# Kernel tuning notes

Measured on AMD Instinct MI355X. Metric: run time of the kernel, lower is better.

The kernel has to match this reference:

```python
import jax, jax.numpy as jnp
import numpy as np

H_HEADS = 4

def setup_inputs() -> dict:
    key = jax.random.key(0)
    ks = jax.random.split(key, 14)
    B, C, H, W = 8, 512, 32, 32
    r = C // H_HEADS  # SE reduction = h per SelfModule(channel, h)
    s_in = 0.02
    inp = {
        'x': jax.random.normal(ks[0], (B, C, H, W), jnp.float32),
        'wq': jax.random.normal(ks[1], (C, C), jnp.float32) * s_in,
        'bq': jnp.zeros((C,), jnp.float32),
        'wk': jax.random.normal(ks[2], (C, C), jnp.float32) * s_in,
        'bk': jnp.zeros((C,), jnp.float32),
        'wv': jax.random.normal(ks[3], (C, C), jnp.float32) * s_in,
        'bv': jnp.zeros((C,), jnp.float32),
        'fc1_w': jax.random.normal(ks[4], (r, C), jnp.float32) * s_in,
        'fc1_b': jnp.zeros((r,), jnp.float32),
        'fc2_w': jax.random.normal(ks[5], (C, r), jnp.float32) * s_in,
        'fc2_b': jnp.zeros((C,), jnp.float32),
        'gate_w': jax.random.normal(ks[6], (1, C), jnp.float32) * s_in,
        'gate_b': jnp.zeros((1,), jnp.float32),
    }
    return inp

def _conv1x1(y, w, b):
    # y: [B,C,H,W], w: [O,C] (1x1 conv kernel squeezed), b: [O]
    return jnp.einsum('bchw,oc->bohw', y, w) + b[None, :, None, None]

def reference(x, wq, bq, wk, bk, wv, bv, fc1_w, fc1_b, fc2_w, fc2_b, gate_w, gate_b):
    B, C, H, W = x.shape
    h = H_HEADS
    dk = C // h
    N = H * W

    # --- SelfScaling (SE without final sigmoid-in-block; sigmoid applied at mul) ---
    p = x.mean(axis=(2, 3))                                   # [B,C] global avg pool
    f = jax.nn.relu(p @ fc1_w.T + fc1_b) @ fc2_w.T + fc2_b    # [B,C]
    x = x * jax.nn.sigmoid(f)[:, :, None, None] + x

    # --- RTrans: conv1x1 QKV, attention over flattened H*W ---
    q = _conv1x1(x, wq, bq).reshape(B, h, dk, N).transpose(0, 1, 3, 2)  # [B,h,N,dk]
    k = _conv1x1(x, wk, bk).reshape(B, h, dk, N)                        # [B,h,dk,N]
    v = _conv1x1(x, wv, bv).reshape(B, h, dk, N)                        # [B,h,dk,N]
    scale = 1.0 / float(np.sqrt(dk))
    att = jax.nn.softmax(jnp.einsum('bhnd,bhdm->bhnm', q, k) * scale, axis=-1)  # [B,h,N,N]
    o = jnp.einsum('bhdn,bhnm->bhdm', v, att).reshape(B, C, H, W)  # v @ att as in torch

    # --- SelfGating ---
    gate = jax.nn.sigmoid(_conv1x1(o, gate_w, gate_b))  # [B,1,H,W]
    return o * gate + o
```

## Files before the change

### kernel.cpp

```cpp
#include <hip/hip_runtime.h>
#include <hip/hip_bf16.h>

#define B_ 8
#define C_ 512
#define N_ 1024
#define HEADS_ 4
#define DK_ 128
#define R_ 128

typedef float f32x4 __attribute__((ext_vector_type(4)));
typedef __bf16 bf16x8 __attribute__((ext_vector_type(8)));
typedef short short4v __attribute__((ext_vector_type(4)));
typedef unsigned short u16;

constexpr float kScale = 0.08838834764831845f;

#define OFF_P   0u
#define OFF_SS  16384u
#define OFF_WB  32768u
#define OFF_XT  1605632u
#define OFF_QT  9994240u
#define OFF_KT  18382848u
#define OFF_V   26771456u
#define OFF_DEN 35160064u
#define OFF_G   35291136u
#define OFF_O1  35323904u
#define OFF_E   52101120u

__device__ __forceinline__ u16 f2b(float f) {
  __hip_bfloat16 h = __float2bfloat16(f);
  return __builtin_bit_cast(u16, h);
}
__device__ __forceinline__ float b2f(u16 u) {
  return __builtin_bit_cast(float, (unsigned)u << 16);
}

typedef const __attribute__((address_space(1))) unsigned int* gptr_t;
typedef __attribute__((address_space(3))) unsigned int* lptr_t;
__device__ __forceinline__ void gload16(const void* g, void* l) {
  __builtin_amdgcn_global_load_lds((gptr_t)g, (lptr_t)l, 16, 0, 0);
}

__device__ __forceinline__ f32x4 mfma16(bf16x8 a, bf16x8 b, f32x4 c) {
  return __builtin_amdgcn_mfma_f32_16x16x32_bf16(a, b, c, 0, 0, 0);
}

__global__ __launch_bounds__(64) void k_pool(const float* __restrict__ x,
                                             float* __restrict__ p) {
  int bc = blockIdx.x, lane = threadIdx.x;
  const float4* row = (const float4*)(x + (size_t)bc * N_);
  float s = 0.f;
  for (int i = lane; i < N_ / 4; i += 64) {
    float4 t = row[i];
    s += t.x + t.y + t.z + t.w;
  }
  for (int o = 32; o > 0; o >>= 1) s += __shfl_down(s, o, 64);
  if (lane == 0) p[bc] = s * (1.0f / N_);
}

__global__ __launch_bounds__(256) void k_se(const float* __restrict__ p,
                                            const float* __restrict__ fc1w,
                                            const float* __restrict__ fc1b,
                                            const float* __restrict__ fc2w,
                                            const float* __restrict__ fc2b,
                                            float* __restrict__ ss) {
  __shared__ float pl[C_];
  __shared__ float f1[R_];
  int b = blockIdx.x, t = threadIdx.x;
  for (int c = t; c < C_; c += 256) pl[c] = p[b * C_ + c];
  __syncthreads();
  if (t < R_) {
    float a = fc1b[t];
    for (int c = 0; c < C_; c++) a += pl[c] * fc1w[t * C_ + c];
    f1[t] = fmaxf(a, 0.f);
  }
  __syncthreads();
  for (int c = t; c < C_; c += 256) {
    float a = fc2b[c];
    for (int j = 0; j < R_; j++) a += f1[j] * fc2w[c * R_ + j];
    ss[b * C_ + c] = 1.f + 1.f / (1.f + __expf(-a));
  }
}

__global__ __launch_bounds__(256) void k_castw_zero(const float* __restrict__ wq,
                                                    const float* __restrict__ wk,
                                                    const float* __restrict__ wv,
                                                    u16* __restrict__ wb,
                                                    float* __restrict__ g) {
  int bid = blockIdx.x;
  if (bid >= 768) {
    g[(bid - 768) * 256 + threadIdx.x] = 0.f;
    return;
  }
  int i = bid * 256 + threadIdx.x;
  int idx = i * 4;
  const float* srcs[3] = {wq, wk, wv};
  int w = idx / (C_ * C_), off = idx % (C_ * C_);
  float4 v = *(const float4*)(srcs[w] + off);
  u16* d = wb + idx;
  d[0] = f2b(v.x); d[1] = f2b(v.y); d[2] = f2b(v.z); d[3] = f2b(v.w);
}

__global__ __launch_bounds__(256) void k_xt(const float* __restrict__ x,
                                            const float* __restrict__ ss,
                                            u16* __restrict__ xt) {
  int b = blockIdx.z, c0 = blockIdx.y * 64, n0 = blockIdx.x * 64;
  __shared__ float tile[64][65];
  int t = threadIdx.x;
  int cr = t >> 4, nc4 = (t & 15) * 4;
  for (int j = 0; j < 4; j++) {
    int c = cr + j * 16;
    float sc = ss[b * C_ + c0 + c];
    float4 v = *(const float4*)(x + ((size_t)b * C_ + c0 + c) * N_ + n0 + nc4);
    tile[c][nc4 + 0] = v.x * sc;
    tile[c][nc4 + 1] = v.y * sc;
    tile[c][nc4 + 2] = v.z * sc;
    tile[c][nc4 + 3] = v.w * sc;
  }
  __syncthreads();
  int nr = t >> 2, cc = (t & 3) * 16;
  u16 ov[16];
  for (int m = 0; m < 16; m++) ov[m] = f2b(tile[cc + m][nr]);
  u16* dst = xt + ((size_t)b * N_ + n0 + nr) * C_ + c0 + cc;
  for (int m = 0; m < 16; m++) dst[m] = ov[m];
}

__global__ __launch_bounds__(256) void k_qkv(const u16* __restrict__ xt,
                                             const u16* __restrict__ wb,
                                             const float* __restrict__ bq,
                                             const float* __restrict__ bk,
                                             const float* __restrict__ bv,
                                             u16* __restrict__ qt,
                                             u16* __restrict__ kt,
                                             u16* __restrict__ v) {
  __shared__ char smem[32768];
  int b = blockIdx.y / 3, sel = blockIdx.y % 3;
  int tile = blockIdx.x;
  const char *Ab, *Bb;
  u16* out;
  const float* bias;
  int mt, nt, rstride;
  size_t xtoff = (size_t)b * N_ * C_;
  if (sel < 2) {
    mt = tile & 7; nt = tile >> 3;
    Ab = (const char*)(xt + xtoff + (size_t)mt * 128 * C_);
    Bb = (const char*)(wb + (size_t)sel * C_ * C_ + (size_t)nt * 128 * C_);
    out = (sel ? kt : qt) + xtoff;
    bias = sel ? bk : bq;
    rstride = C_ * 2;
  } else {
    mt = tile & 3; nt = tile >> 2;
    Ab = (const char*)(wb + (size_t)2 * C_ * C_ + (size_t)mt * 128 * C_);
    Bb = (const char*)(xt + xtoff + (size_t)nt * 128 * C_);
    out = v + (size_t)b * C_ * N_;
    bias = bv;
    rstride = N_ * 2;
  }
  int t = threadIdx.x, lane = t & 63, wid = t >> 6;
  int wr = wid >> 1, wc = wid & 1;
  const f32x4 z4 = {0.f, 0.f, 0.f, 0.f};
  f32x4 acc[4][4];
  for (int i = 0; i < 4; i++)
    for (int j = 0; j < 4; j++) acc[i][j] = z4;

  char* lA = smem;
  char* lB = smem + 16384;
  for (int ko = 0; ko < C_; ko += 64) {
    __syncthreads();
    for (int i = wid; i < 16; i += 4) {
      int beta = i * 1024 + lane * 16;
      int row = beta >> 7, cb = (beta & 127) ^ ((row & 7) << 4);
      gload16(Ab + (size_t)row * 1024 + ko * 2 + cb, lA + beta);
    }
    for (int i = wid; i < 16; i += 4) {
      int beta = i * 1024 + lane * 16;
      int row = beta >> 7, cb = (beta & 127) ^ ((row & 7) << 4);
      gload16(Bb + (size_t)row * 1024 + ko * 2 + cb, lB + beta);
    }
    __syncthreads();
    for (int ks = 0; ks < 2; ks++) {
      int kb = ks * 64 + (lane >> 4) * 16;
      bf16x8 af[4], bfr[4];
      for (int fi = 0; fi < 4; fi++) {
        int row = wr * 64 + fi * 16 + (lane & 15);
        af[fi] = *(const bf16x8*)(lA + row * 128 + (kb ^ ((row & 7) << 4)));
      }
      for (int fj = 0; fj < 4; fj++) {
        int row = wc * 64 + fj * 16 + (lane & 15);
        bfr[fj] = *(const bf16x8*)(lB + row * 128 + (kb ^ ((row & 7) << 4)));
      }
      for (int fi = 0; fi < 4; fi++)
        for (int fj = 0; fj < 4; fj++)
          acc[fi][fj] = mfma16(af[fi], bfr[fj], acc[fi][fj]);
    }
  }
  __syncthreads();
  for (int fi = 0; fi < 4; fi++)
    for (int fj = 0; fj < 4; fj++) {
      int colb = wc * 64 + fj * 16 + (lane & 15);
      for (int r = 0; r < 4; r++) {
        int rowb = wr * 64 + fi * 16 + (lane >> 4) * 4 + r;
        float bva = (sel < 2) ? bias[nt * 128 + colb] : bias[mt * 128 + rowb];
        float val = acc[fi][fj][r] + bva;
        int byte = rowb * 256 + ((colb * 2) ^ ((rowb & 7) << 4));
        *(u16*)(smem + byte) = f2b(val);
      }
    }
  __syncthreads();
  for (int i = t; i < 2048; i += 256) {
    int row = i >> 4, cb = (i & 15) * 16;
    bf16x8 val = *(const bf16x8*)(smem + row * 256 + (cb ^ ((row & 7) << 4)));
    *(bf16x8*)((char*)out + (size_t)(mt * 128 + row) * rstride + nt * 256 + cb) = val;
  }
}

__global__ __launch_bounds__(256) void k_passA(const u16* __restrict__ qt,
                                               const u16* __restrict__ kt,
                                               u16* __restrict__ et,
                                               float* __restrict__ invden) {
  __shared__ char lK[2][32768];
  __shared__ char lE[16384];
  int bh = blockIdx.x, nb = blockIdx.y * 64;
  int b = bh >> 2, h = bh & 3;
  const char* qb = (const char*)(qt + (size_t)b * N_ * C_ + h * DK_);
  const char* kb = (const char*)(kt + (size_t)b * N_ * C_ + h * DK_);
  char* etb = (char*)(et + (size_t)bh * N_ * N_);
  int t = threadIdx.x, lane = t & 63, wid = t >> 6;
  bf16x8 bq[4];
  {
    const char* qr = qb + (size_t)(nb + wid * 16 + (lane & 15)) * (C_ * 2);
    for (int ks = 0; ks < 4; ks++)
      bq[ks] = *(const bf16x8*)(qr + ks * 64 + (lane >> 4) * 16);
  }
  float dpart = 0.f;
  const f32x4 z4 = {0.f, 0.f, 0.f, 0.f};
  for (int i = wid; i < 32; i += 4) {
    int beta = i * 1024 + lane * 16;
    int row = beta >> 8, cb = (beta & 255) ^ ((row & 15) << 4);
    gload16(kb + (size_t)row * (C_ * 2) + cb, lK[0] + beta);
  }
  int nloc2 = (wid * 16 + (lane & 15)) * 2;
  for (int mc = 0; mc < 8; mc++) {
    int cur = mc & 1;
    __syncthreads();
    if (mc < 7) {
      int mnext = (mc + 1) * 128;
      for (int i = wid; i < 32; i += 4) {
        int beta = i * 1024 + lane * 16;
        int row = beta >> 8, cb = (beta & 255) ^ ((row & 15) << 4);
        gload16(kb + (size_t)(mnext + row) * (C_ * 2) + cb, lK[cur ^ 1] + beta);
      }
    }
    for (int fj = 0; fj < 8; fj++) {
      f32x4 s = z4;
      for (int ks = 0; ks < 4; ks++) {
        int row = fj * 16 + (lane & 15);
        bf16x8 ak = *(const bf16x8*)(lK[cur] + row * 256 +
                                     ((ks * 64 + (lane >> 4) * 16) ^ ((row & 15) << 4)));
        s = mfma16(ak, bq[ks], s);
      }
      for (int r = 0; r < 4; r++) {
        float e = __expf(s[r] * kScale);
        dpart += e;
        int m = fj * 16 + (lane >> 4) * 4 + r;
        *(u16*)(lE + m * 128 + (nloc2 ^ ((m & 7) << 4))) = f2b(e);
      }
    }
    __syncthreads();
    for (int i = t; i < 1024; i += 256) {
      int row = i >> 3, c16 = (i & 7) * 16;
      bf16x8 val = *(const bf16x8*)(lE + row * 128 + (c16 ^ ((row & 7) << 4)));
      *(bf16x8*)(etb + (size_t)(mc * 128 + row) * (N_ * 2) + nb * 2 + c16) = val;
    }
  }
  dpart += __shfl_xor(dpart, 16, 64);
  dpart += __shfl_xor(dpart, 32, 64);
  if (lane < 16)
    invden[(size_t)bh * N_ + nb + wid * 16 + lane] = 1.f / dpart;
}

__global__ __launch_bounds__(256) void k_vscale(u16* __restrict__ v,
                                                const float* __restrict__ invden) {
  size_t i = ((size_t)blockIdx.x * 256 + threadIdx.x) * 8;
  int n = (int)(i & (N_ - 1));
  int bc = (int)(i >> 10);
  int b = bc >> 9, c = bc & 511, h = c >> 7;
  const float* iv = invden + ((size_t)(b * 4 + h)) * N_ + n;
  float4 iv0 = *(const float4*)(iv);
  float4 iv1 = *(const float4*)(iv + 4);
  u16* p = v + i;
  short4v a = *(short4v*)p, bb = *(short4v*)(p + 4);
  u16 o[8];
  o[0] = f2b(b2f((u16)a[0]) * iv0.x);
  o[1] = f2b(b2f((u16)a[1]) * iv0.y);
  o[2] = f2b(b2f((u16)a[2]) * iv0.z);
  o[3] = f2b(b2f((u16)a[3]) * iv0.w);
  o[4] = f2b(b2f((u16)bb[0]) * iv1.x);
  o[5] = f2b(b2f((u16)bb[1]) * iv1.y);
  o[6] = f2b(b2f((u16)bb[2]) * iv1.z);
  o[7] = f2b(b2f((u16)bb[3]) * iv1.w);
  short4v r0 = {(short)o[0], (short)o[1], (short)o[2], (short)o[3]};
  short4v r1 = {(short)o[4], (short)o[5], (short)o[6], (short)o[7]};
  *(short4v*)p = r0;
  *(short4v*)(p + 4) = r1;
}

__global__ __launch_bounds__(256) void k_passB(const u16* __restrict__ v,
                                               const u16* __restrict__ et,
                                               const float* __restrict__ gw,
                                               float* __restrict__ out0,
                                               float* __restrict__ o1,
                                               float* __restrict__ g) {
  __shared__ char smem[32768];
  __shared__ float gacc[128];
  int bh = blockIdx.x, mt = blockIdx.y, nh = blockIdx.z;
  int b = bh >> 2, h = bh & 3;
  const char* Ab = (const char*)(v + ((size_t)b * C_ + h * DK_) * N_) + nh * 1024;
  const char* Bb = (const char*)(et + (size_t)bh * N_ * N_ + (size_t)mt * 128 * N_) + nh * 1024;
  float* ob = (nh ? o1 : out0) + ((size_t)b * C_ + h * DK_) * N_ + mt * 128;
  int t = threadIdx.x, lane = t & 63, wid = t >> 6;
  int wr = wid >> 1, wc = wid & 1;
  if (t < 128) gacc[t] = 0.f;
  const f32x4 z4 = {0.f, 0.f, 0.f, 0.f};
  f32x4 acc[4][4];
  for (int i = 0; i < 4; i++)
    for (int j = 0; j < 4; j++) acc[i][j] = z4;

  char* lA = smem;
  char* lB = smem + 16384;
  for (int ko = 0; ko < 512; ko += 64) {
    __syncthreads();
    for (int i = wid; i < 16; i += 4) {
      int beta = i * 1024 + lane * 16;
      int row = beta >> 7, cb = (beta & 127) ^ ((row & 7) << 4);
      gload16(Ab + (size_t)row * 2048 + ko * 2 + cb, lA + beta);
    }
    for (int i = wid; i < 16; i += 4) {
      int beta = i * 1024 + lane * 16;
      int row = beta >> 7, cb = (beta & 127) ^ ((row & 7) << 4);
      gload16(Bb + (size_t)row * 2048 + ko * 2 + cb, lB + beta);
    }
    __syncthreads();
    for (int ks = 0; ks < 2; ks++) {
      int kb = ks * 64 + (lane >> 4) * 16;
      bf16x8 af[4], bfr[4];
      for (int fi = 0; fi < 4; fi++) {
        int row = wr * 64 + fi * 16 + (lane & 15);
        af[fi] = *(const bf16x8*)(lA + row * 128 + (kb ^ ((row & 7) << 4)));
      }
      for (int fj = 0; fj < 4; fj++) {
        int row = wc * 64 + fj * 16 + (lane & 15);
        bfr[fj] = *(const bf16x8*)(lB + row * 128 + (kb ^ ((row & 7) << 4)));
      }
      for (int fi = 0; fi < 4; fi++)
        for (int fj = 0; fj < 4; fj++)
          acc[fi][fj] = mfma16(af[fi], bfr[fj], acc[fi][fj]);
    }
  }
  for (int fj = 0; fj < 4; fj++) {
    int mcol = wc * 64 + fj * 16 + (lane & 15);
    float part = 0.f;
    for (int fi = 0; fi < 4; fi++) {
      int d = wr * 64 + fi * 16 + (lane >> 4) * 4;
      float4 gwv = *(const float4*)(gw + h * DK_ + d);
      float ga[4] = {gwv.x, gwv.y, gwv.z, gwv.w};
      for (int r = 0; r < 4; r++) {
        float val = acc[fi][fj][r];
        ob[(size_t)(d + r) * N_ + mcol] = val;
        part += ga[r] * val;
      }
    }
    atomicAdd(&gacc[mcol], part);
  }
  __syncthreads();
  if (t < 128) atomicAdd(&g[(size_t)b * N_ + mt * 128 + t], gacc[t]);
}

__global__ __launch_bounds__(256) void k_gate_apply(const float* __restrict__ g,
                                                    const float* __restrict__ gb,
                                                    const float* __restrict__ o1,
                                                    float* __restrict__ out) {
  size_t i = ((size_t)blockIdx.x * 256 + threadIdx.x) * 4;
  int b = (int)(i / ((size_t)C_ * N_));
  int n = (int)(i & (N_ - 1));
  float4 gv = *(const float4*)(g + (size_t)b * N_ + n);
  float bias = gb[0];
  float4 v0 = *(float4*)(out + i);
  float4 v1 = *(const float4*)(o1 + i);
  float ox = v0.x + v1.x, oy = v0.y + v1.y, oz = v0.z + v1.z, ow = v0.w + v1.w;
  ox *= 1.f + 1.f / (1.f + __expf(-(gv.x + bias)));
  oy *= 1.f + 1.f / (1.f + __expf(-(gv.y + bias)));
  oz *= 1.f + 1.f / (1.f + __expf(-(gv.z + bias)));
  ow *= 1.f + 1.f / (1.f + __expf(-(gv.w + bias)));
  float4 r = {ox, oy, oz, ow};
  *(float4*)(out + i) = r;
}

extern "C" void kernel_launch(void* const* d_in, const int* in_sizes, int n_in,
                              void* d_out, int out_size, void* d_ws, size_t ws_size,
                              hipStream_t stream) {
  const float* x    = (const float*)d_in[0];
  const float* wq   = (const float*)d_in[1];
  const float* bq   = (const float*)d_in[2];
  const float* wk   = (const float*)d_in[3];
  const float* bk   = (const float*)d_in[4];
  const float* wv   = (const float*)d_in[5];
  const float* bv   = (const float*)d_in[6];
  const float* fc1w = (const float*)d_in[7];
  const float* fc1b = (const float*)d_in[8];
  const float* fc2w = (const float*)d_in[9];
  const float* fc2b = (const float*)d_in[10];
  const float* gw   = (const float*)d_in[11];
  const float* gb   = (const float*)d_in[12];
  float* out = (float*)d_out;
  char* ws = (char*)d_ws;

  float* p   = (float*)(ws + OFF_P);
  float* ssc = (float*)(ws + OFF_SS);
  u16* wb  = (u16*)(ws + OFF_WB);
  u16* xt  = (u16*)(ws + OFF_XT);
  u16* qt  = (u16*)(ws + OFF_QT);
  u16* kt  = (u16*)(ws + OFF_KT);
  u16* v   = (u16*)(ws + OFF_V);
  float* den = (float*)(ws + OFF_DEN);
  float* g   = (float*)(ws + OFF_G);
  float* o1  = (float*)(ws + OFF_O1);
  u16* et  = (u16*)(ws + OFF_E);

  k_pool<<<B_ * C_, 64, 0, stream>>>(x, p);
  k_castw_zero<<<800, 256, 0, stream>>>(wq, wk, wv, wb, g);
  k_se<<<B_, 256, 0, stream>>>(p, fc1w, fc1b, fc2w, fc2b, ssc);
  k_xt<<<dim3(16, 8, B_), 256, 0, stream>>>(x, ssc, xt);
  k_qkv<<<dim3(32, B_ * 3), 256, 0, stream>>>(xt, wb, bq, bk, bv, qt, kt, v);
  k_passA<<<dim3(32, 16), 256, 0, stream>>>(qt, kt, et, den);
  k_vscale<<<2048, 256, 0, stream>>>(v, den);
  k_passB<<<dim3(32, 8, 2), 256, 0, stream>>>(v, et, gw, out, o1, g);
  k_gate_apply<<<B_ * C_ * N_ / 1024, 256, 0, stream>>>(g, gb, o1, out);
}
```

Baseline: 120.3 us.

## Split passA over key halves with atomic denominator accumulation; vectorize xt stores

```diff
diff --git a/kernel.cpp b/kernel.cpp
--- a/kernel.cpp
+++ b/kernel.cpp
@@ -11,6 +11,7 @@
 typedef float f32x4 __attribute__((ext_vector_type(4)));
 typedef __bf16 bf16x8 __attribute__((ext_vector_type(8)));
 typedef short short4v __attribute__((ext_vector_type(4)));
+typedef short short8v __attribute__((ext_vector_type(8)));
 typedef unsigned short u16;
 
 constexpr float kScale = 0.08838834764831845f;
@@ -86,8 +87,13 @@
                                                     const float* __restrict__ wk,
                                                     const float* __restrict__ wv,
                                                     u16* __restrict__ wb,
-                                                    float* __restrict__ g) {
+                                                    float* __restrict__ g,
+                                                    float* __restrict__ den) {
   int bid = blockIdx.x;
+  if (bid >= 800) {
+    den[(bid - 800) * 256 + threadIdx.x] = 0.f;
+    return;
+  }
   if (bid >= 768) {
     g[(bid - 768) * 256 + threadIdx.x] = 0.f;
     return;
@@ -119,10 +125,14 @@
   }
   __syncthreads();
   int nr = t >> 2, cc = (t & 3) * 16;
-  u16 ov[16];
-  for (int m = 0; m < 16; m++) ov[m] = f2b(tile[cc + m][nr]);
+  short8v s0, s1;
+  for (int m = 0; m < 8; m++) {
+    s0[m] = (short)f2b(tile[cc + m][nr]);
+    s1[m] = (short)f2b(tile[cc + 8 + m][nr]);
+  }
   u16* dst = xt + ((size_t)b * N_ + n0 + nr) * C_ + c0 + cc;
-  for (int m = 0; m < 16; m++) dst[m] = ov[m];
+  *(short8v*)dst = s0;
+  *(short8v*)(dst + 8) = s1;
 }
 
 __global__ __launch_bounds__(256) void k_qkv(const u16* __restrict__ xt,
@@ -217,10 +227,10 @@
 __global__ __launch_bounds__(256) void k_passA(const u16* __restrict__ qt,
                                                const u16* __restrict__ kt,
                                                u16* __restrict__ et,
-                                               float* __restrict__ invden) {
-  __shared__ char lK[2][32768];
-  __shared__ char lE[16384];
-  int bh = blockIdx.x, nb = blockIdx.y * 64;
+                                               float* __restrict__ den) {
+  __shared__ char lK[2][16384];
+  __shared__ char lE[8192];
+  int bh = blockIdx.x, nb = blockIdx.y * 64, mh = blockIdx.z;
   int b = bh >> 2, h = bh & 3;
   const char* qb = (const char*)(qt + (size_t)b * N_ * C_ + h * DK_);
   const char* kb = (const char*)(kt + (size_t)b * N_ * C_ + h * DK_);
@@ -234,24 +244,25 @@
   }
   float dpart = 0.f;
   const f32x4 z4 = {0.f, 0.f, 0.f, 0.f};
-  for (int i = wid; i < 32; i += 4) {
+  int m0 = mh * 512;
+  for (int i = wid; i < 16; i += 4) {
     int beta = i * 1024 + lane * 16;
     int row = beta >> 8, cb = (beta & 255) ^ ((row & 15) << 4);
-    gload16(kb + (size_t)row * (C_ * 2) + cb, lK[0] + beta);
+    gload16(kb + (size_t)(m0 + row) * (C_ * 2) + cb, lK[0] + beta);
   }
   int nloc2 = (wid * 16 + (lane & 15)) * 2;
   for (int mc = 0; mc < 8; mc++) {
     int cur = mc & 1;
     __syncthreads();
     if (mc < 7) {
-      int mnext = (mc + 1) * 128;
-      for (int i = wid; i < 32; i += 4) {
+      int mnext = m0 + (mc + 1) * 64;
+      for (int i = wid; i < 16; i += 4) {
         int beta = i * 1024 + lane * 16;
         int row = beta >> 8, cb = (beta & 255) ^ ((row & 15) << 4);
         gload16(kb + (size_t)(mnext + row) * (C_ * 2) + cb, lK[cur ^ 1] + beta);
       }
     }
-    for (int fj = 0; fj < 8; fj++) {
+    for (int fj = 0; fj < 4; fj++) {
       f32x4 s = z4;
       for (int ks = 0; ks < 4; ks++) {
         int row = fj * 16 + (lane & 15);
@@ -267,38 +278,38 @@
       }
     }
     __syncthreads();
-    for (int i = t; i < 1024; i += 256) {
+    for (int i = t; i < 512; i += 256) {
       int row = i >> 3, c16 = (i & 7) * 16;
       bf16x8 val = *(const bf16x8*)(lE + row * 128 + (c16 ^ ((row & 7) << 4)));
-      *(bf16x8*)(etb + (size_t)(mc * 128 + row) * (N_ * 2) + nb * 2 + c16) = val;
+      *(bf16x8*)(etb + (size_t)(m0 + mc * 64 + row) * (N_ * 2) + nb * 2 + c16) = val;
     }
   }
   dpart += __shfl_xor(dpart, 16, 64);
   dpart += __shfl_xor(dpart, 32, 64);
   if (lane < 16)
-    invden[(size_t)bh * N_ + nb + wid * 16 + lane] = 1.f / dpart;
+    atomicAdd(&den[(size_t)bh * N_ + nb + wid * 16 + lane], dpart);
 }
 
 __global__ __launch_bounds__(256) void k_vscale(u16* __restrict__ v,
-                                                const float* __restrict__ invden) {
+                                                const float* __restrict__ den) {
   size_t i = ((size_t)blockIdx.x * 256 + threadIdx.x) * 8;
   int n = (int)(i & (N_ - 1));
   int bc = (int)(i >> 10);
   int b = bc >> 9, c = bc & 511, h = c >> 7;
-  const float* iv = invden + ((size_t)(b * 4 + h)) * N_ + n;
-  float4 iv0 = *(const float4*)(iv);
-  float4 iv1 = *(const float4*)(iv + 4);
+  const float* dv = den + ((size_t)(b * 4 + h)) * N_ + n;
+  float4 d0 = *(const float4*)(dv);
+  float4 d1 = *(const float4*)(dv + 4);
   u16* p = v + i;
   short4v a = *(short4v*)p, bb = *(short4v*)(p + 4);
   u16 o[8];
-  o[0] = f2b(b2f((u16)a[0]) * iv0.x);
-  o[1] = f2b(b2f((u16)a[1]) * iv0.y);
-  o[2] = f2b(b2f((u16)a[2]) * iv0.z);
-  o[3] = f2b(b2f((u16)a[3]) * iv0.w);
-  o[4] = f2b(b2f((u16)bb[0]) * iv1.x);
-  o[5] = f2b(b2f((u16)bb[1]) * iv1.y);
-  o[6] = f2b(b2f((u16)bb[2]) * iv1.z);
-  o[7] = f2b(b2f((u16)bb[3]) * iv1.w);
+  o[0] = f2b(b2f((u16)a[0]) / d0.x);
+  o[1] = f2b(b2f((u16)a[1]) / d0.y);
+  o[2] = f2b(b2f((u16)a[2]) / d0.z);
+  o[3] = f2b(b2f((u16)a[3]) / d0.w);
+  o[4] = f2b(b2f((u16)bb[0]) / d1.x);
+  o[5] = f2b(b2f((u16)bb[1]) / d1.y);
+  o[6] = f2b(b2f((u16)bb[2]) / d1.z);
+  o[7] = f2b(b2f((u16)bb[3]) / d1.w);
   short4v r0 = {(short)o[0], (short)o[1], (short)o[2], (short)o[3]};
   short4v r1 = {(short)o[4], (short)o[5], (short)o[6], (short)o[7]};
   *(short4v*)p = r0;
@@ -428,11 +439,11 @@
   u16* et  = (u16*)(ws + OFF_E);
 
   k_pool<<<B_ * C_, 64, 0, stream>>>(x, p);
-  k_castw_zero<<<800, 256, 0, stream>>>(wq, wk, wv, wb, g);
+  k_castw_zero<<<928, 256, 0, stream>>>(wq, wk, wv, wb, g, den);
   k_se<<<B_, 256, 0, stream>>>(p, fc1w, fc1b, fc2w, fc2b, ssc);
   k_xt<<<dim3(16, 8, B_), 256, 0, stream>>>(x, ssc, xt);
   k_qkv<<<dim3(32, B_ * 3), 256, 0, stream>>>(xt, wb, bq, bk, bv, qt, kt, v);
-  k_passA<<<dim3(32, 16), 256, 0, stream>>>(qt, kt, et, den);
+  k_passA<<<dim3(32, 16, 2), 256, 0, stream>>>(qt, kt, et, den);
   k_vscale<<<2048, 256, 0, stream>>>(v, den);
   k_passB<<<dim3(32, 8, 2), 256, 0, stream>>>(v, et, gw, out, o1, g);
   k_gate_apply<<<B_ * C_ * N_ / 1024, 256, 0, stream>>>(g, gb, o1, out);
```

Measured after the change: 119.5 us. No clear change (-0.7%).
